# Optimization experiments

Hardware: AMD Instinct MI355X
Metric: run time of the kernel (lower is better)

The kernel has to match this reference:

```python
import jax, jax.numpy as jnp
import numpy as np

H_DIM = 2048
D_FF = 4 * H_DIM
NUM_EXPERTS = 8
NUM_SHARED = 2
BATCH, SEQ = 2, 2048


def setup_inputs() -> dict:
    key = jax.random.key(0)
    ks = jax.random.split(key, 10)
    s = 0.02
    return {
        "x": jax.random.normal(ks[0], (BATCH, SEQ, H_DIM), dtype=jnp.float32),
        "ws_w1": jax.random.normal(ks[1], (NUM_SHARED, H_DIM, D_FF), dtype=jnp.float32) * s,
        "ws_b1": jnp.zeros((NUM_SHARED, D_FF), dtype=jnp.float32),
        "ws_w2": jax.random.normal(ks[2], (NUM_SHARED, D_FF, H_DIM), dtype=jnp.float32) * s,
        "ws_b2": jnp.zeros((NUM_SHARED, H_DIM), dtype=jnp.float32),
        "we_w1": jax.random.normal(ks[3], (NUM_EXPERTS, H_DIM, D_FF), dtype=jnp.float32) * s,
        "we_b1": jnp.zeros((NUM_EXPERTS, D_FF), dtype=jnp.float32),
        "we_w2": jax.random.normal(ks[4], (NUM_EXPERTS, D_FF, H_DIM), dtype=jnp.float32) * s,
        "we_b2": jnp.zeros((NUM_EXPERTS, H_DIM), dtype=jnp.float32),
        "wg": jax.random.normal(ks[5], (H_DIM, NUM_EXPERTS), dtype=jnp.float32) * s,
        "top_k": 2,
    }


def reference(x, ws_w1, ws_b1, ws_w2, ws_b2, we_w1, we_b1, we_w2, we_b2, wg, top_k):
    B, S, D = x.shape
    xt = x.reshape(-1, D)  # [T, D], T = B*S
    T = xt.shape[0]

    # ---- shared experts: sum over NUM_SHARED dense MLPs ----
    hs = jax.nn.relu(jnp.einsum('td,ndf->ntf', xt, ws_w1) + ws_b1[:, None, :])
    shared = jnp.einsum('ntf,nfd->td', hs, ws_w2) + ws_b2.sum(axis=0)  # [T, D]

    # ---- sparse top-k routed MoE ----
    logits = xt @ wg                       # [T, E] router logits
    probs = jax.nn.softmax(logits, axis=-1)
    topv, topi = jax.lax.top_k(probs, top_k)
    gates = jnp.zeros_like(probs).at[jnp.arange(T)[:, None], topi].set(topv)  # [T, E]

    moe = jnp.zeros_like(xt)
    for e in range(we_w1.shape[0]):  # small fixed expert count
        he = jax.nn.relu(xt @ we_w1[e] + we_b1[e])
        ye = he @ we_w2[e] + we_b2[e]
        moe = moe + gates[:, e:e + 1] * ye

    out = (shared + moe).reshape(B, S, D)
    return out, logits
```

## Files before the change

### kernel.cpp

```cpp
#include <hip/hip_runtime.h>

#define TOKENS 4096
#define HD 2048
#define FF 8192
#define NE 8
#define NS 2

typedef __attribute__((ext_vector_type(8))) short bf16x8;
typedef __attribute__((ext_vector_type(4))) float f32x4;

__device__ __forceinline__ unsigned rnd_bf(unsigned u) {
  return u + 0x7fffu + ((u >> 16) & 1u);
}
__device__ __forceinline__ unsigned short f2bf(float f) {
  unsigned u = __builtin_bit_cast(unsigned, f);
  return (unsigned short)(rnd_bf(u) >> 16);
}

#define GLDS16(gp, lp)                                                         \
  __builtin_amdgcn_global_load_lds(                                            \
      (const __attribute__((address_space(1))) unsigned*)(const void*)(gp),    \
      (__attribute__((address_space(3))) unsigned*)(lp), 16, 0, 0)

__global__ void cast_x_kernel(const float* __restrict__ x, unsigned short* __restrict__ xb) {
  const size_t i = ((size_t)blockIdx.x * 256 + threadIdx.x) * 4;
  float4 v = *(const float4*)(x + i);
  ushort4 o;
  o.x = f2bf(v.x); o.y = f2bf(v.y); o.z = f2bf(v.z); o.w = f2bf(v.w);
  *(ushort4*)(xb + i) = o;
}

__global__ void router_kernel(const float* __restrict__ x, const float* __restrict__ wg,
                              float* __restrict__ logits_out, int* __restrict__ topi,
                              float* __restrict__ topv, int* __restrict__ counts) {
  const int wave = threadIdx.x >> 6, lane = threadIdx.x & 63;
  const int t = blockIdx.x * 4 + wave;
  const float* xr = x + (size_t)t * HD;
  float acc[8];
#pragma unroll
  for (int e = 0; e < 8; ++e) acc[e] = 0.f;
  for (int d = lane; d < HD; d += 64) {
    const float xv = xr[d];
    const float4 w0 = *(const float4*)(wg + (size_t)d * 8);
    const float4 w1 = *(const float4*)(wg + (size_t)d * 8 + 4);
    acc[0] += xv * w0.x; acc[1] += xv * w0.y; acc[2] += xv * w0.z; acc[3] += xv * w0.w;
    acc[4] += xv * w1.x; acc[5] += xv * w1.y; acc[6] += xv * w1.z; acc[7] += xv * w1.w;
  }
#pragma unroll
  for (int e = 0; e < 8; ++e) {
#pragma unroll
    for (int off = 32; off > 0; off >>= 1) acc[e] += __shfl_xor(acc[e], off);
  }
  if (lane == 0) {
    *(float4*)(logits_out + (size_t)t * 8)     = make_float4(acc[0], acc[1], acc[2], acc[3]);
    *(float4*)(logits_out + (size_t)t * 8 + 4) = make_float4(acc[4], acc[5], acc[6], acc[7]);
    float mx = acc[0];
#pragma unroll
    for (int e = 1; e < 8; ++e) mx = fmaxf(mx, acc[e]);
    float p[8], s = 0.f;
#pragma unroll
    for (int e = 0; e < 8; ++e) { p[e] = expf(acc[e] - mx); s += p[e]; }
    const float inv = 1.f / s;
    int i1 = 0;
#pragma unroll
    for (int e = 1; e < 8; ++e) if (acc[e] > acc[i1]) i1 = e;
    int i2 = (i1 == 0) ? 1 : 0;
#pragma unroll
    for (int e = 0; e < 8; ++e) if (e != i1 && acc[e] > acc[i2]) i2 = e;
    topi[2 * t]     = i1; topv[2 * t]     = p[i1] * inv;
    topi[2 * t + 1] = i2; topv[2 * t + 1] = p[i2] * inv;
    atomicAdd(&counts[i1], 1);
    atomicAdd(&counts[i2], 1);
  }
}

__global__ void offs_kernel(const int* __restrict__ counts, int* __restrict__ offs,
                            int* __restrict__ cursors) {
  if (threadIdx.x == 0) {
    int r = 0;
    for (int e = 0; e < NE; ++e) { offs[e] = r; cursors[e] = r; r += counts[e]; }
  }
}

__global__ void gather_kernel(const unsigned short* __restrict__ xb,
                              const int* __restrict__ topi, const float* __restrict__ topv,
                              int* __restrict__ cursors, unsigned short* __restrict__ xg,
                              int* __restrict__ row_token, float* __restrict__ row_gate) {
  const int wave = threadIdx.x >> 6, lane = threadIdx.x & 63;
  const int t = blockIdx.x * 4 + wave;
  const uint4* src = (const uint4*)(xb + (size_t)t * HD);
#pragma unroll
  for (int j = 0; j < 2; ++j) {
    const int e = topi[2 * t + j];
    int pos = 0;
    if (lane == 0) {
      pos = atomicAdd(&cursors[e], 1);
      row_token[pos] = t;
      row_gate[pos] = topv[2 * t + j];
    }
    pos = __shfl(pos, 0);
    uint4* dst = (uint4*)(xg + (size_t)pos * HD);
#pragma unroll
    for (int c = lane; c < 256; c += 64) dst[c] = src[c];
  }
}

template <int K, int N>
__global__ __launch_bounds__(256) void pack_wt(const float* __restrict__ we,
                                               const float* __restrict__ ws,
                                               unsigned short* __restrict__ dstw) {
  const int e = blockIdx.z;
  const float* src = (e < NE) ? (we + (size_t)e * K * N) : (ws + (size_t)(e - NE) * K * N);
  unsigned short* dst = dstw + (size_t)e * K * N;
  const int nt = blockIdx.x * 64;
  const int kt = blockIdx.y * 64;
  __shared__ unsigned short t[64][73];
  const int tid = threadIdx.x;
  const int rr = tid >> 4, cc = (tid & 15) * 4;
#pragma unroll
  for (int i = 0; i < 4; ++i) {
    const int k = rr + i * 16;
    float4 v = *(const float4*)(src + (size_t)(kt + k) * N + nt + cc);
    t[k][cc + 0] = f2bf(v.x);
    t[k][cc + 1] = f2bf(v.y);
    t[k][cc + 2] = f2bf(v.z);
    t[k][cc + 3] = f2bf(v.w);
  }
  __syncthreads();
  const int nr = tid >> 2, kc = (tid & 3) * 16;
  unsigned u[8];
#pragma unroll
  for (int j = 0; j < 8; ++j)
    u[j] = (unsigned)t[kc + 2 * j][nr] | ((unsigned)t[kc + 2 * j + 1][nr] << 16);
  unsigned short* dp = dst + (size_t)(nt + nr) * K + kt + kc;
  uint4 v0; v0.x = u[0]; v0.y = u[1]; v0.z = u[2]; v0.w = u[3];
  uint4 v1; v1.x = u[4]; v1.y = u[5]; v1.z = u[6]; v1.w = u[7];
  *(uint4*)dp = v0;
  *(uint4*)(dp + 8) = v1;
}

template <int MODE>
__global__ __launch_bounds__(256) void gemm_bt(
    const unsigned short* __restrict__ Ash,
    const unsigned short* __restrict__ Art,
    const unsigned short* __restrict__ wt,
    const float* __restrict__ bE, const float* __restrict__ bS,
    unsigned short* __restrict__ hout, float* __restrict__ out,
    const int* __restrict__ counts, const int* __restrict__ offs,
    const int* __restrict__ row_token, const float* __restrict__ row_gate) {
  constexpr int K = (MODE == 0) ? HD : FF;
  constexpr int N = (MODE == 0) ? FF : HD;
  constexpr int NBLK = N / 128;
  constexpr int NWG = NBLK * 32;

  const int e = blockIdx.z;
  int M;
  const unsigned short* A;
  const float* bias;
  int hbase = 0;
  const int* tok = nullptr;
  const float* gt = nullptr;

  if (e < NE) {
    M = counts[e];
    const int off = offs[e];
    A = Art + (size_t)off * K;
    if (MODE == 1) { tok = row_token + off; gt = row_gate + off; }
    bias = bE + (size_t)e * N;
    hbase = off;
  } else {
    M = TOKENS;
    const int se = e - NE;
    hbase = 2 * TOKENS + se * TOKENS;
    if (MODE == 0) A = Ash;
    else           A = Ash + (size_t)hbase * K;
    bias = bS + (size_t)se * N;
  }
  const unsigned short* Bt = wt + (size_t)e * HD * FF;

  int flat = blockIdx.x + NBLK * blockIdx.y;
  flat = (flat & 7) * (NWG >> 3) + (flat >> 3);
  const int m0 = (flat & 31) * 128;
  const int n0 = (flat >> 5) * 128;
  if (m0 >= M) return;

  __shared__ __align__(16) unsigned short As[128 * 64];
  __shared__ __align__(16) unsigned short Bs[128 * 64];

  const int tid = threadIdx.x;
  const int wv = tid >> 6;
  const int ln = tid & 63;
  const int fr = ln & 15;
  const int fq = ln >> 4;
  const int wr = (wv >> 1) * 64;
  const int wc = (wv & 1) * 64;
  const int lrow = ln >> 3;
  const int lcs = ((ln & 7) ^ lrow) << 3;

  f32x4 acc[4][4];
#pragma unroll
  for (int i = 0; i < 4; ++i)
#pragma unroll
    for (int j = 0; j < 4; ++j) acc[i][j] = (f32x4){0.f, 0.f, 0.f, 0.f};

  const unsigned short* a_base = A + (size_t)(m0 + wv * 32 + lrow) * K + lcs;
  const unsigned short* b_base = Bt + (size_t)(n0 + wv * 32 + lrow) * K + lcs;
  unsigned short* as_base = As + (wv * 32) * 64;
  unsigned short* bs_base = Bs + (wv * 32) * 64;

  const int nkt = K / 64;
  for (int kt = 0; kt < nkt; ++kt) {
    const int ko = kt * 64;
#pragma unroll
    for (int i = 0; i < 4; ++i)
      GLDS16(a_base + (size_t)(i * 8) * K + ko, as_base + (i * 8) * 64);
#pragma unroll
    for (int i = 0; i < 4; ++i)
      GLDS16(b_base + (size_t)(i * 8) * K + ko, bs_base + (i * 8) * 64);
    __syncthreads();
#pragma unroll
    for (int kk = 0; kk < 2; ++kk) {
      bf16x8 af[4], bfr[4];
#pragma unroll
      for (int mi = 0; mi < 4; ++mi) {
        const int row = wr + mi * 16 + fr;
        af[mi] = *(const bf16x8*)(As + row * 64 + ((kk * 32 + fq * 8) ^ ((row & 7) << 3)));
      }
#pragma unroll
      for (int ni = 0; ni < 4; ++ni) {
        const int col = wc + ni * 16 + fr;
        bfr[ni] = *(const bf16x8*)(Bs + col * 64 + ((kk * 32 + fq * 8) ^ ((col & 7) << 3)));
      }
#pragma unroll
      for (int mi = 0; mi < 4; ++mi)
#pragma unroll
        for (int ni = 0; ni < 4; ++ni)
          acc[mi][ni] = __builtin_amdgcn_mfma_f32_16x16x32_bf16(af[mi], bfr[ni], acc[mi][ni], 0, 0, 0);
    }
    __syncthreads();
  }

  if (MODE == 0) {
#pragma unroll
    for (int ni = 0; ni < 4; ++ni) {
      const int col = n0 + wc + ni * 16 + fr;
      const float bb = bias[col];
#pragma unroll
      for (int mi = 0; mi < 4; ++mi) {
#pragma unroll
        for (int j = 0; j < 4; ++j) {
          const int r = m0 + wr + mi * 16 + fq * 4 + j;
          if (r < M) {
            float v = acc[mi][ni][j] + bb;
            v = v > 0.f ? v : 0.f;
            hout[(size_t)(hbase + r) * FF + col] = f2bf(v);
          }
        }
      }
    }
  } else {
#pragma unroll
    for (int mi = 0; mi < 4; ++mi) {
#pragma unroll
      for (int j = 0; j < 4; ++j) {
        const int r = m0 + wr + mi * 16 + fq * 4 + j;
        if (r < M) {
          const int t = tok ? tok[r] : r;
          const float g = gt ? gt[r] : 1.f;
          float* orow = out + (size_t)t * HD + n0;
#pragma unroll
          for (int ni = 0; ni < 4; ++ni) {
            const int col = wc + ni * 16 + fr;
            atomicAdd(orow + col, g * (acc[mi][ni][j] + bias[n0 + col]));
          }
        }
      }
    }
  }
}

extern "C" void kernel_launch(void* const* d_in, const int* in_sizes, int n_in,
                              void* d_out, int out_size, void* d_ws, size_t ws_size,
                              hipStream_t stream) {
  const float* x     = (const float*)d_in[0];
  const float* ws_w1 = (const float*)d_in[1];
  const float* ws_b1 = (const float*)d_in[2];
  const float* ws_w2 = (const float*)d_in[3];
  const float* ws_b2 = (const float*)d_in[4];
  const float* we_w1 = (const float*)d_in[5];
  const float* we_b1 = (const float*)d_in[6];
  const float* we_w2 = (const float*)d_in[7];
  const float* we_b2 = (const float*)d_in[8];
  const float* wg    = (const float*)d_in[9];

  float* out = (float*)d_out;
  float* logits = out + (size_t)TOKENS * HD;

  char* ws = (char*)d_ws;
  unsigned short* wt   = (unsigned short*)ws;
  unsigned short* hbuf = (unsigned short*)(ws + 335544320);
  unsigned short* xb   = (unsigned short*)(ws + 603979776);
  unsigned short* xg   = (unsigned short*)(ws + 620756992);
  char* ctrl = ws + 654835712;
  int*   row_token = (int*)(ctrl);
  float* row_gate  = (float*)(ctrl + 32768);
  int*   topi      = (int*)(ctrl + 65536);
  float* topv      = (float*)(ctrl + 98304);
  int*   counts    = (int*)(ctrl + 131072);
  int*   offs      = (int*)(ctrl + 131104);
  int*   cursors   = (int*)(ctrl + 131136);

  hipMemsetAsync(out, 0, (size_t)TOKENS * HD * sizeof(float), stream);
  hipMemsetAsync(counts, 0, NE * sizeof(int), stream);

  cast_x_kernel<<<8192, 256, 0, stream>>>(x, xb);
  router_kernel<<<1024, 256, 0, stream>>>(x, wg, logits, topi, topv, counts);
  offs_kernel<<<1, 64, 0, stream>>>(counts, offs, cursors);
  gather_kernel<<<1024, 256, 0, stream>>>(xb, topi, topv, cursors, xg, row_token, row_gate);

  pack_wt<HD, FF><<<dim3(FF / 64, HD / 64, 10), 256, 0, stream>>>(we_w1, ws_w1, wt);
  gemm_bt<0><<<dim3(64, 32, 10), 256, 0, stream>>>(
      xb, xg, wt, we_b1, ws_b1, hbuf, nullptr, counts, offs, nullptr, nullptr);
  pack_wt<FF, HD><<<dim3(HD / 64, FF / 64, 10), 256, 0, stream>>>(we_w2, ws_w2, wt);
  gemm_bt<1><<<dim3(16, 32, 10), 256, 0, stream>>>(
      hbuf, hbuf, wt, we_b2, ws_b2, nullptr, out, counts, offs, row_token, row_gate);

  (void)in_sizes; (void)n_in; (void)out_size; (void)ws_size;
}
```

Before: 2.165 ms.

## Replace GEMM with 256x256-tile, 8-wave, double-buffered pipelined kernel

```diff
diff --git a/kernel.cpp b/kernel.cpp
--- a/kernel.cpp
+++ b/kernel.cpp
@@ -139,8 +139,43 @@
   *(uint4*)(dp + 8) = v1;
 }
 
+template <int MS>
+__device__ __forceinline__ void rd_a(bf16x8 (&d)[8], const unsigned short* base,
+                                     int wr, int fr, int fq, int swz) {
+#pragma unroll
+  for (int mi = 0; mi < 4; ++mi)
+#pragma unroll
+    for (int ks = 0; ks < 2; ++ks)
+      d[mi * 2 + ks] = *(const bf16x8*)(base + (wr * 128 + MS * 64 + mi * 16 + fr) * 64 +
+                                        (((ks * 4 + fq) ^ swz) << 3));
+}
+template <int NSUB>
+__device__ __forceinline__ void rd_b(bf16x8 (&d)[4], const unsigned short* base,
+                                     int wc, int fr, int fq, int swz) {
+#pragma unroll
+  for (int ni = 0; ni < 2; ++ni)
+#pragma unroll
+    for (int ks = 0; ks < 2; ++ks)
+      d[ni * 2 + ks] = *(const bf16x8*)(base + (wc * 64 + NSUB * 32 + ni * 16 + fr) * 64 +
+                                        (((ks * 4 + fq) ^ swz) << 3));
+}
+template <int MS, int NSUB>
+__device__ __forceinline__ void mm16(f32x4 (&acc)[8][4], const bf16x8 (&a)[8],
+                                     const bf16x8 (&b)[4]) {
+  __builtin_amdgcn_s_setprio(1);
+#pragma unroll
+  for (int mi = 0; mi < 4; ++mi)
+#pragma unroll
+    for (int ni = 0; ni < 2; ++ni)
+#pragma unroll
+      for (int ks = 0; ks < 2; ++ks)
+        acc[MS * 4 + mi][NSUB * 2 + ni] = __builtin_amdgcn_mfma_f32_16x16x32_bf16(
+            a[mi * 2 + ks], b[ni * 2 + ks], acc[MS * 4 + mi][NSUB * 2 + ni], 0, 0, 0);
+  __builtin_amdgcn_s_setprio(0);
+}
+
 template <int MODE>
-__global__ __launch_bounds__(256) void gemm_bt(
+__global__ __launch_bounds__(512, 2) void gemm8p(
     const unsigned short* __restrict__ Ash,
     const unsigned short* __restrict__ Art,
     const unsigned short* __restrict__ wt,
@@ -150,8 +185,9 @@
     const int* __restrict__ row_token, const float* __restrict__ row_gate) {
   constexpr int K = (MODE == 0) ? HD : FF;
   constexpr int N = (MODE == 0) ? FF : HD;
-  constexpr int NBLK = N / 128;
-  constexpr int NWG = NBLK * 32;
+  constexpr int NBX = N / 256;
+  constexpr int NWG = NBX * 16;
+  extern __shared__ unsigned short smem[];
 
   const int e = blockIdx.z;
   int M;
@@ -178,80 +214,89 @@
   }
   const unsigned short* Bt = wt + (size_t)e * HD * FF;
 
-  int flat = blockIdx.x + NBLK * blockIdx.y;
+  int flat = blockIdx.x + NBX * blockIdx.y;
   flat = (flat & 7) * (NWG >> 3) + (flat >> 3);
-  const int m0 = (flat & 31) * 128;
-  const int n0 = (flat >> 5) * 128;
+  const int m0 = (flat & 15) * 256;
+  const int n0 = (flat >> 4) * 256;
   if (m0 >= M) return;
 
-  __shared__ __align__(16) unsigned short As[128 * 64];
-  __shared__ __align__(16) unsigned short Bs[128 * 64];
-
   const int tid = threadIdx.x;
-  const int wv = tid >> 6;
-  const int ln = tid & 63;
-  const int fr = ln & 15;
-  const int fq = ln >> 4;
-  const int wr = (wv >> 1) * 64;
-  const int wc = (wv & 1) * 64;
-  const int lrow = ln >> 3;
-  const int lcs = ((ln & 7) ^ lrow) << 3;
-
-  f32x4 acc[4][4];
-#pragma unroll
-  for (int i = 0; i < 4; ++i)
+  const int wid = tid >> 6, ln = tid & 63;
+  const int wr = wid >> 2, wc = wid & 3;
+  const int fr = ln & 15, fq = ln >> 4;
+  const int swz = fr & 7;
+
+  const int srr = tid >> 3;
+  const int soct = tid & 7;
+  const int scol = (soct ^ (srr & 7)) << 3;
+
+#define STAGE_A(h, kt, b)                                                      \
+  { const unsigned short* s_ = A + (size_t)(m0 + (h) * 128 + srr) * K + (kt) * 64 + scol; \
+    unsigned short* d_ = smem + (b) * 32768 + ((h) * 128 + srr) * 64 + soct * 8; \
+    GLDS16(s_, d_); GLDS16(s_ + (size_t)64 * K, d_ + 4096); }
+#define STAGE_B(h, kt, b)                                                      \
+  { const unsigned short* s_ = Bt + (size_t)(n0 + (h) * 128 + srr) * K + (kt) * 64 + scol; \
+    unsigned short* d_ = smem + (b) * 32768 + 16384 + ((h) * 128 + srr) * 64 + soct * 8; \
+    GLDS16(s_, d_); GLDS16(s_ + (size_t)64 * K, d_ + 4096); }
+
+  f32x4 acc[8][4];
+#pragma unroll
+  for (int i = 0; i < 8; ++i)
 #pragma unroll
     for (int j = 0; j < 4; ++j) acc[i][j] = (f32x4){0.f, 0.f, 0.f, 0.f};
 
-  const unsigned short* a_base = A + (size_t)(m0 + wv * 32 + lrow) * K + lcs;
-  const unsigned short* b_base = Bt + (size_t)(n0 + wv * 32 + lrow) * K + lcs;
-  unsigned short* as_base = As + (wv * 32) * 64;
-  unsigned short* bs_base = Bs + (wv * 32) * 64;
-
+  STAGE_A(0, 0, 0); STAGE_B(0, 0, 0); STAGE_A(1, 0, 0); STAGE_B(1, 0, 0);
+  STAGE_B(0, 1, 1); STAGE_A(0, 1, 1);
+  asm volatile("s_waitcnt vmcnt(4)" ::: "memory");
+  __builtin_amdgcn_s_barrier();
+
+  bf16x8 a0[8], a1[8], b0[4], b1[4];
   const int nkt = K / 64;
-  for (int kt = 0; kt < nkt; ++kt) {
-    const int ko = kt * 64;
-#pragma unroll
-    for (int i = 0; i < 4; ++i)
-      GLDS16(a_base + (size_t)(i * 8) * K + ko, as_base + (i * 8) * 64);
-#pragma unroll
-    for (int i = 0; i < 4; ++i)
-      GLDS16(b_base + (size_t)(i * 8) * K + ko, bs_base + (i * 8) * 64);
-    __syncthreads();
-#pragma unroll
-    for (int kk = 0; kk < 2; ++kk) {
-      bf16x8 af[4], bfr[4];
-#pragma unroll
-      for (int mi = 0; mi < 4; ++mi) {
-        const int row = wr + mi * 16 + fr;
-        af[mi] = *(const bf16x8*)(As + row * 64 + ((kk * 32 + fq * 8) ^ ((row & 7) << 3)));
-      }
-#pragma unroll
-      for (int ni = 0; ni < 4; ++ni) {
-        const int col = wc + ni * 16 + fr;
-        bfr[ni] = *(const bf16x8*)(Bs + col * 64 + ((kk * 32 + fq * 8) ^ ((col & 7) << 3)));
-      }
-#pragma unroll
-      for (int mi = 0; mi < 4; ++mi)
-#pragma unroll
-        for (int ni = 0; ni < 4; ++ni)
-          acc[mi][ni] = __builtin_amdgcn_mfma_f32_16x16x32_bf16(af[mi], bfr[ni], acc[mi][ni], 0, 0, 0);
-    }
-    __syncthreads();
-  }
+  int cur = 0;
+  for (int t = 0; t < nkt; ++t) {
+    const int nxt = cur ^ 1;
+    const int tp1 = (t + 1 < nkt) ? t + 1 : t;
+    const int tp2 = (t + 2 < nkt) ? t + 2 : t;
+    const unsigned short* As_c = smem + cur * 32768;
+    const unsigned short* Bs_c = As_c + 16384;
+    rd_a<0>(a0, As_c, wr, fr, fq, swz);
+    rd_b<0>(b0, Bs_c, wc, fr, fq, swz);
+    STAGE_A(1, tp1, nxt);
+    __builtin_amdgcn_s_barrier();
+    mm16<0, 0>(acc, a0, b0);
+    __builtin_amdgcn_s_barrier();
+    rd_b<1>(b1, Bs_c, wc, fr, fq, swz);
+    STAGE_B(1, tp1, nxt);
+    __builtin_amdgcn_s_barrier();
+    mm16<0, 1>(acc, a0, b1);
+    __builtin_amdgcn_s_barrier();
+    rd_a<1>(a1, As_c, wr, fr, fq, swz);
+    STAGE_B(0, tp2, cur);
+    __builtin_amdgcn_s_barrier();
+    mm16<1, 1>(acc, a1, b1);
+    __builtin_amdgcn_s_barrier();
+    STAGE_A(0, tp2, cur);
+    __builtin_amdgcn_s_barrier();
+    mm16<1, 0>(acc, a1, b0);
+    asm volatile("s_waitcnt vmcnt(4)" ::: "memory");
+    __builtin_amdgcn_s_barrier();
+    cur = nxt;
+  }
+#undef STAGE_A
+#undef STAGE_B
 
   if (MODE == 0) {
 #pragma unroll
-    for (int ni = 0; ni < 4; ++ni) {
-      const int col = n0 + wc + ni * 16 + fr;
+    for (int nn = 0; nn < 4; ++nn) {
+      const int col = n0 + wc * 64 + (nn >> 1) * 32 + (nn & 1) * 16 + fr;
       const float bb = bias[col];
 #pragma unroll
-      for (int mi = 0; mi < 4; ++mi) {
+      for (int mm = 0; mm < 8; ++mm) {
 #pragma unroll
         for (int j = 0; j < 4; ++j) {
-          const int r = m0 + wr + mi * 16 + fq * 4 + j;
+          const int r = m0 + wr * 128 + (mm >> 2) * 64 + (mm & 3) * 16 + fq * 4 + j;
           if (r < M) {
-            float v = acc[mi][ni][j] + bb;
+            float v = acc[mm][nn][j] + bb;
             v = v > 0.f ? v : 0.f;
             hout[(size_t)(hbase + r) * FF + col] = f2bf(v);
           }
@@ -260,18 +305,18 @@
     }
   } else {
 #pragma unroll
-    for (int mi = 0; mi < 4; ++mi) {
+    for (int mm = 0; mm < 8; ++mm) {
 #pragma unroll
       for (int j = 0; j < 4; ++j) {
-        const int r = m0 + wr + mi * 16 + fq * 4 + j;
+        const int r = m0 + wr * 128 + (mm >> 2) * 64 + (mm & 3) * 16 + fq * 4 + j;
         if (r < M) {
           const int t = tok ? tok[r] : r;
           const float g = gt ? gt[r] : 1.f;
           float* orow = out + (size_t)t * HD + n0;
 #pragma unroll
-          for (int ni = 0; ni < 4; ++ni) {
-            const int col = wc + ni * 16 + fr;
-            atomicAdd(orow + col, g * (acc[mi][ni][j] + bias[n0 + col]));
+          for (int nn = 0; nn < 4; ++nn) {
+            const int col = wc * 64 + (nn >> 1) * 32 + (nn & 1) * 16 + fr;
+            atomicAdd(orow + col, g * (acc[mm][nn][j] + bias[n0 + col]));
           }
         }
       }
@@ -298,9 +343,9 @@
 
   char* ws = (char*)d_ws;
   unsigned short* wt   = (unsigned short*)ws;
-  unsigned short* hbuf = (unsigned short*)(ws + 335544320);
-  unsigned short* xb   = (unsigned short*)(ws + 603979776);
-  unsigned short* xg   = (unsigned short*)(ws + 620756992);
+  unsigned short* xb   = (unsigned short*)(ws + 335544320);
+  unsigned short* xg   = (unsigned short*)(ws + 352321536);
+  unsigned short* hbuf = (unsigned short*)(ws + 386400256);
   char* ctrl = ws + 654835712;
   int*   row_token = (int*)(ctrl);
   float* row_gate  = (float*)(ctrl + 32768);
@@ -310,6 +355,11 @@
   int*   offs      = (int*)(ctrl + 131104);
   int*   cursors   = (int*)(ctrl + 131136);
 
+  hipFuncSetAttribute(reinterpret_cast<const void*>(gemm8p<0>),
+                      hipFuncAttributeMaxDynamicSharedMemorySize, 131072);
+  hipFuncSetAttribute(reinterpret_cast<const void*>(gemm8p<1>),
+                      hipFuncAttributeMaxDynamicSharedMemorySize, 131072);
+
   hipMemsetAsync(out, 0, (size_t)TOKENS * HD * sizeof(float), stream);
   hipMemsetAsync(counts, 0, NE * sizeof(int), stream);
 
@@ -319,10 +369,10 @@
   gather_kernel<<<1024, 256, 0, stream>>>(xb, topi, topv, cursors, xg, row_token, row_gate);
 
   pack_wt<HD, FF><<<dim3(FF / 64, HD / 64, 10), 256, 0, stream>>>(we_w1, ws_w1, wt);
-  gemm_bt<0><<<dim3(64, 32, 10), 256, 0, stream>>>(
+  gemm8p<0><<<dim3(32, 16, 10), 512, 131072, stream>>>(
       xb, xg, wt, we_b1, ws_b1, hbuf, nullptr, counts, offs, nullptr, nullptr);
   pack_wt<FF, HD><<<dim3(HD / 64, FF / 64, 10), 256, 0, stream>>>(we_w2, ws_w2, wt);
-  gemm_bt<1><<<dim3(16, 32, 10), 256, 0, stream>>>(
+  gemm8p<1><<<dim3(8, 16, 10), 512, 131072, stream>>>(
       hbuf, hbuf, wt, we_b2, ws_b2, nullptr, out, counts, offs, row_token, row_gate);
 
   (void)in_sizes; (void)n_in; (void)out_size; (void)ws_size;
```

New measurement: 2.019 ms. 1.07x faster.
